# Optimization experiments

Hardware: AMD Instinct MI355X
Metric: run time of the kernel (lower is better)

Reference implementation:

```python
import jax, jax.numpy as jnp
import numpy as np

B, A, T, NMODE, H = 4, 16, 32, 8, 256
NSCENE = 512
HEADS = 8
FF = 128
LN_EPS = 1e-6

def _layer_norm(x, g, b, eps=LN_EPS):
    mu = jnp.mean(x, axis=-1, keepdims=True)
    var = jnp.mean((x - mu) ** 2, axis=-1, keepdims=True)
    return (x - mu) * jax.lax.rsqrt(var + eps) * g + b


def setup_inputs() -> dict:
    key = jax.random.key(0)
    ks = jax.random.split(key, 16)
    s = 1.0 / np.sqrt(H)
    sf = 1.0 / np.sqrt(FF)
    return {
        "hidden_vecs": jax.random.normal(ks[0], (B, A, T, NMODE, H), jnp.float32),
        "scene_hidden_vec": jax.random.normal(ks[1], (B, NSCENE, H), jnp.float32),
        # nn.MultiheadAttention packed in_proj: rows [Wq; Wk; Wv]
        "in_proj_w": jax.random.normal(ks[2], (3 * H, H), jnp.float32) * s,
        "in_proj_b": jnp.zeros((3 * H,), jnp.float32),
        "out_proj_w": jax.random.normal(ks[3], (H, H), jnp.float32) * s,
        "out_proj_b": jnp.zeros((H,), jnp.float32),
        "attn_ln_g": jnp.ones((H,), jnp.float32),
        "attn_ln_b": jnp.zeros((H,), jnp.float32),
        "ff1_w": jax.random.normal(ks[4], (FF, H), jnp.float32) * s,
        "ff1_b": jnp.zeros((FF,), jnp.float32),
        "ff2_w": jax.random.normal(ks[5], (H, FF), jnp.float32) * sf,
        "ff2_b": jnp.zeros((H,), jnp.float32),
        "ff_ln_g": jnp.ones((H,), jnp.float32),
        "ff_ln_b": jnp.zeros((H,), jnp.float32),
    }


def reference(hidden_vecs, scene_hidden_vec, in_proj_w, in_proj_b, out_proj_w,
              out_proj_b, attn_ln_g, attn_ln_b, ff1_w, ff1_b, ff2_w, ff2_b,
              ff_ln_g, ff_ln_b):
    b, a, t, n, h = hidden_vecs.shape
    N = scene_hidden_vec.shape[1]
    d = h // HEADS
    m = a * t * n  # queries per batch element

    Wq, Wk, Wv = in_proj_w[:h], in_proj_w[h:2 * h], in_proj_w[2 * h:]
    bq, bk, bv = in_proj_b[:h], in_proj_b[h:2 * h], in_proj_b[2 * h:]

    # Project queries; K/V computed ONCE per batch (shared across a,t,n) --
    # avoids materializing the (b,a,t,n,N,h) expanded tensor.
    q = (hidden_vecs.reshape(b, m, h) @ Wq.T + bq).reshape(b, m, HEADS, d)
    k = (scene_hidden_vec @ Wk.T + bk).reshape(b, N, HEADS, d)
    v = (scene_hidden_vec @ Wv.T + bv).reshape(b, N, HEADS, d)

    scale = 1.0 / np.sqrt(d)
    scores = jnp.einsum('bmed,bned->bemn', q * scale, k)  # (b, heads, m, N)
    attn = jax.nn.softmax(scores, axis=-1)
    ctx = jnp.einsum('bemn,bned->bmed', attn, v).reshape(b, m, h)
    attn_out = (ctx @ out_proj_w.T + out_proj_b).reshape(b, a, t, n, h)

    # averaged attention weights over heads (average_attn_weights=True)
    attn_score = jnp.mean(attn, axis=1).reshape(b, a, t, n, 1, N)

    x = _layer_norm(attn_out + hidden_vecs, attn_ln_g, attn_ln_b)
    ff = jax.nn.relu(x @ ff1_w.T + ff1_b) @ ff2_w.T + ff2_b
    out = _layer_norm(ff + x, ff_ln_g, ff_ln_b)
    return out, attn_score
```

## Files before the change

### kernel.cpp

```cpp
#include <hip/hip_runtime.h>
#include <hip/hip_bf16.h>

#define H 256
#define NSC 512
#define MQ 4096
#define BATCH 4

typedef __attribute__((ext_vector_type(8))) short bf16x8;
typedef __attribute__((ext_vector_type(4))) float f32x4;

__device__ __forceinline__ ushort f2bf(float x) {
    union { float f; unsigned u; } c; c.f = x;
    unsigned r = c.u + 0x7FFF + ((c.u >> 16) & 1);
    return (ushort)(r >> 16);
}
__device__ __forceinline__ unsigned pk2(float hi, float lo) {
    union { float f; unsigned u; } a, b; a.f = hi; b.f = lo;
    return __builtin_amdgcn_perm(a.u, b.u, 0x07060302u);
}
__device__ __forceinline__ uint4 cvt8f(const float* p) {
    float4 a = *(const float4*)p;
    float4 b = *(const float4*)(p + 4);
    uint4 r;
    r.x = pk2(a.y, a.x); r.y = pk2(a.w, a.z);
    r.z = pk2(b.y, b.x); r.w = pk2(b.w, b.z);
    return r;
}
#define EXP2(x) __builtin_amdgcn_exp2f(x)

template<int ATYPE>
__device__ __forceinline__ uint4 load_a(const void* Ain, size_t off) {
    if (ATYPE == 0) return cvt8f((const float*)Ain + off);
    return *(const uint4*)((const ushort*)Ain + off);
}

template<int ATYPE, int MODE>
__global__ __launch_bounds__(512, 4) void gemm_kernel(
    const void* __restrict__ Ain, const float* __restrict__ W,
    const float* __restrict__ bias, const float* __restrict__ res,
    const float* __restrict__ lng, const float* __restrict__ lnb,
    void* __restrict__ out, ushort* __restrict__ out2,
    int K, int N, float alpha, int relu)
{
    __shared__ ushort As[64 * 64];
    __shared__ ushort Bs[256 * 64];
    __shared__ float Ls[64 * 4];
    __shared__ float Lq[64 * 4];
    const int t = threadIdx.x;
    const int w = t >> 6, lane = t & 63, g = lane >> 4, l15 = lane & 15;
    const int rowBase = blockIdx.y * 64;
    const int colBase = blockIdx.x * 256;
    const int wr = (w >> 2) * 32;
    const int wc = (w & 3) * 64;
    f32x4 acc[2][4];
    #pragma unroll
    for (int mt = 0; mt < 2; mt++)
        #pragma unroll
        for (int nt = 0; nt < 4; nt++) acc[mt][nt] = (f32x4){0.f,0.f,0.f,0.f};

    const int sr = t >> 3, skc = t & 7, sp = skc ^ (sr & 7);
    const size_t arow = (size_t)(rowBase + sr) * K + skc * 8;

    uint4 av = load_a<ATYPE>(Ain, arow);
    uint4 bv[4];
    #pragma unroll
    for (int i = 0; i < 4; i++) {
        const int u = t + 512*i, br = u >> 3, bkc = u & 7;
        int brow = colBase + br; if (brow > N - 1) brow = N - 1;
        bv[i] = cvt8f(W + (size_t)brow * K + bkc*8);
    }

    for (int k0 = 0; k0 < K; k0 += 64) {
        __syncthreads();
        *(uint4*)&As[sr*64 + sp*8] = av;
        #pragma unroll
        for (int i = 0; i < 4; i++) {
            const int u = t + 512*i, br = u >> 3, bkc = u & 7, bp = bkc ^ (br & 7);
            *(uint4*)&Bs[br*64 + bp*8] = bv[i];
        }
        __syncthreads();
        if (k0 + 64 < K) {
            av = load_a<ATYPE>(Ain, arow + k0 + 64);
            #pragma unroll
            for (int i = 0; i < 4; i++) {
                const int u = t + 512*i, br = u >> 3, bkc = u & 7;
                int brow = colBase + br; if (brow > N - 1) brow = N - 1;
                bv[i] = cvt8f(W + (size_t)brow * K + k0 + 64 + bkc*8);
            }
        }
        #pragma unroll
        for (int kk = 0; kk < 2; kk++) {
            const int swz = ((kk*4 + g) ^ (l15 & 7)) * 8;
            bf16x8 af[2], bfr[4];
            #pragma unroll
            for (int mt = 0; mt < 2; mt++)
                af[mt] = *(const bf16x8*)&As[(wr + mt*16 + l15)*64 + swz];
            #pragma unroll
            for (int nt = 0; nt < 4; nt++)
                bfr[nt] = *(const bf16x8*)&Bs[(wc + nt*16 + l15)*64 + swz];
            #pragma unroll
            for (int mt = 0; mt < 2; mt++)
                #pragma unroll
                for (int nt = 0; nt < 4; nt++)
                    acc[mt][nt] = __builtin_amdgcn_mfma_f32_16x16x32_bf16(
                        af[mt], bfr[nt], acc[mt][nt], 0, 0, 0);
        }
    }

    if (MODE == 0) {
        #pragma unroll
        for (int nt = 0; nt < 4; nt++) {
            const int col = colBase + wc + nt*16 + l15;
            if (col < N) {
                const float bb = bias[col];
                #pragma unroll
                for (int mt = 0; mt < 2; mt++)
                    #pragma unroll
                    for (int r = 0; r < 4; r++) {
                        const int row = rowBase + wr + mt*16 + g*4 + r;
                        float o = (acc[mt][nt][r] + bb) * alpha;
                        if (relu) o = fmaxf(o, 0.f);
                        ((ushort*)out)[(size_t)row * N + col] = f2bf(o);
                    }
            }
        }
    } else if (MODE == 1) {
        #pragma unroll
        for (int nt = 0; nt < 4; nt++) {
            const int col = colBase + wc + nt*16 + l15;
            const float bb = bias[col];
            #pragma unroll
            for (int mt = 0; mt < 2; mt++) {
                const int row0 = rowBase + wr + mt*16 + g*4;
                if (col < 256) {
                    #pragma unroll
                    for (int r = 0; r < 4; r++)
                        ((ushort*)out)[(size_t)(row0 + r) * 256 + col] = f2bf(acc[mt][nt][r] + bb);
                } else {
                    ushort4 pkv = { f2bf(acc[mt][nt][0] + bb), f2bf(acc[mt][nt][1] + bb),
                                    f2bf(acc[mt][nt][2] + bb), f2bf(acc[mt][nt][3] + bb) };
                    *(ushort4*)&out2[(size_t)((row0 >> 9)*256 + col - 256) * 512 + (row0 & 511)] = pkv;
                }
            }
        }
    } else {
        float bb[4], gmv[4], btv[4];
        #pragma unroll
        for (int nt = 0; nt < 4; nt++) {
            const int col = wc + nt*16 + l15;
            bb[nt] = bias[col]; gmv[nt] = lng[col]; btv[nt] = lnb[col];
        }
        #pragma unroll
        for (int mt = 0; mt < 2; mt++)
            #pragma unroll
            for (int r = 0; r < 4; r++) {
                const int row = rowBase + wr + mt*16 + g*4 + r;
                const float* rp = res + (size_t)row * 256;
                #pragma unroll
                for (int nt = 0; nt < 4; nt++)
                    acc[mt][nt][r] += bb[nt] + rp[wc + nt*16 + l15];
            }
        float ps[2][4], pq[2][4];
        #pragma unroll
        for (int mt = 0; mt < 2; mt++)
            #pragma unroll
            for (int r = 0; r < 4; r++) {
                float s = (acc[mt][0][r] + acc[mt][1][r]) + (acc[mt][2][r] + acc[mt][3][r]);
                float qq = (acc[mt][0][r]*acc[mt][0][r] + acc[mt][1][r]*acc[mt][1][r])
                         + (acc[mt][2][r]*acc[mt][2][r] + acc[mt][3][r]*acc[mt][3][r]);
                #pragma unroll
                for (int m = 1; m < 16; m <<= 1) {
                    s += __shfl_xor(s, m);
                    qq += __shfl_xor(qq, m);
                }
                ps[mt][r] = s; pq[mt][r] = qq;
            }
        if (l15 == 0) {
            #pragma unroll
            for (int mt = 0; mt < 2; mt++)
                #pragma unroll
                for (int r = 0; r < 4; r++) {
                    const int ri = wr + mt*16 + g*4 + r;
                    Ls[ri*4 + (w & 3)] = ps[mt][r];
                    Lq[ri*4 + (w & 3)] = pq[mt][r];
                }
        }
        __syncthreads();
        #pragma unroll
        for (int mt = 0; mt < 2; mt++)
            #pragma unroll
            for (int r = 0; r < 4; r++) {
                const int ri = wr + mt*16 + g*4 + r;
                const int row = rowBase + ri;
                f32x4 sv = *(const f32x4*)&Ls[ri*4];
                f32x4 qv = *(const f32x4*)&Lq[ri*4];
                const float mu = (sv[0]+sv[1]+sv[2]+sv[3]) * (1.f/256.f);
                const float ex2 = (qv[0]+qv[1]+qv[2]+qv[3]) * (1.f/256.f);
                const float rs = rsqrtf(ex2 - mu*mu + 1e-6f);
                #pragma unroll
                for (int nt = 0; nt < 4; nt++) {
                    const int col = wc + nt*16 + l15;
                    const float o = (acc[mt][nt][r] - mu) * rs * gmv[nt] + btv[nt];
                    ((float*)out)[(size_t)row * 256 + col] = o;
                    if (out2) out2[(size_t)row * 256 + col] = f2bf(o);
                }
            }
    }
}

__global__ __launch_bounds__(512, 2) void ffn_kernel(
    const ushort* __restrict__ ctx, const float* __restrict__ Wo,
    const float* __restrict__ bo, const float* __restrict__ hid,
    const float* __restrict__ ag, const float* __restrict__ ab,
    const float* __restrict__ W1, const float* __restrict__ b1,
    const float* __restrict__ W2, const float* __restrict__ b2,
    const float* __restrict__ fg, const float* __restrict__ fbv,
    float* __restrict__ out)
{
    __shared__ ushort As[64 * 64];
    __shared__ ushort Bs[256 * 64];
    __shared__ ushort Xb[64 * 256];
    __shared__ ushort Fb[64 * 128];
    __shared__ float Ls[64 * 4];
    __shared__ float Lq[64 * 4];

    const int t = threadIdx.x;
    const int w = t >> 6, lane = t & 63, g = lane >> 4, l15 = lane & 15;
    const int rowBase = blockIdx.x * 64;
    const int wr = (w >> 2) * 32;
    const int wc = (w & 3) * 64;
    const int sr = t >> 3, skc = t & 7, sp = skc ^ (sr & 7);

    float xres[2][4][4];

    {
        f32x4 acc[2][4];
        #pragma unroll
        for (int mt = 0; mt < 2; mt++)
            #pragma unroll
            for (int nt = 0; nt < 4; nt++) acc[mt][nt] = (f32x4){0.f,0.f,0.f,0.f};

        uint4 av = *(const uint4*)(ctx + (size_t)(rowBase + sr) * 256 + skc*8);
        uint4 bv[4];
        #pragma unroll
        for (int i = 0; i < 4; i++) {
            const int u = t + 512*i, br = u >> 3, bkc = u & 7;
            bv[i] = cvt8f(Wo + (size_t)br * 256 + bkc*8);
        }
        for (int k0 = 0; k0 < 256; k0 += 64) {
            __syncthreads();
            *(uint4*)&As[sr*64 + sp*8] = av;
            #pragma unroll
            for (int i = 0; i < 4; i++) {
                const int u = t + 512*i, br = u >> 3, bkc = u & 7, bp = bkc ^ (br & 7);
                *(uint4*)&Bs[br*64 + bp*8] = bv[i];
            }
            __syncthreads();
            if (k0 < 192) {
                av = *(const uint4*)(ctx + (size_t)(rowBase + sr) * 256 + k0 + 64 + skc*8);
                #pragma unroll
                for (int i = 0; i < 4; i++) {
                    const int u = t + 512*i, br = u >> 3, bkc = u & 7;
                    bv[i] = cvt8f(Wo + (size_t)br * 256 + k0 + 64 + bkc*8);
                }
            }
            #pragma unroll
            for (int kk = 0; kk < 2; kk++) {
                const int swz = ((kk*4 + g) ^ (l15 & 7)) * 8;
                bf16x8 af[2], bfr[4];
                #pragma unroll
                for (int mt = 0; mt < 2; mt++)
                    af[mt] = *(const bf16x8*)&As[(wr + mt*16 + l15)*64 + swz];
                #pragma unroll
                for (int nt = 0; nt < 4; nt++)
                    bfr[nt] = *(const bf16x8*)&Bs[(wc + nt*16 + l15)*64 + swz];
                #pragma unroll
                for (int mt = 0; mt < 2; mt++)
                    #pragma unroll
                    for (int nt = 0; nt < 4; nt++)
                        acc[mt][nt] = __builtin_amdgcn_mfma_f32_16x16x32_bf16(
                            af[mt], bfr[nt], acc[mt][nt], 0, 0, 0);
            }
        }
        float bb[4], gmv[4], btv[4];
        #pragma unroll
        for (int nt = 0; nt < 4; nt++) {
            const int col = wc + nt*16 + l15;
            bb[nt] = bo[col]; gmv[nt] = ag[col]; btv[nt] = ab[col];
        }
        #pragma unroll
        for (int mt = 0; mt < 2; mt++)
            #pragma unroll
            for (int r = 0; r < 4; r++) {
                const int row = rowBase + wr + mt*16 + g*4 + r;
                const float* rp = hid + (size_t)row * 256;
                #pragma unroll
                for (int nt = 0; nt < 4; nt++)
                    acc[mt][nt][r] += bb[nt] + rp[wc + nt*16 + l15];
            }
        float ps[2][4], pq[2][4];
        #pragma unroll
        for (int mt = 0; mt < 2; mt++)
            #pragma unroll
            for (int r = 0; r < 4; r++) {
                float s = (acc[mt][0][r] + acc[mt][1][r]) + (acc[mt][2][r] + acc[mt][3][r]);
                float qq = (acc[mt][0][r]*acc[mt][0][r] + acc[mt][1][r]*acc[mt][1][r])
                         + (acc[mt][2][r]*acc[mt][2][r] + acc[mt][3][r]*acc[mt][3][r]);
                #pragma unroll
                for (int m = 1; m < 16; m <<= 1) {
                    s += __shfl_xor(s, m);
                    qq += __shfl_xor(qq, m);
                }
                ps[mt][r] = s; pq[mt][r] = qq;
            }
        if (l15 == 0) {
            #pragma unroll
            for (int mt = 0; mt < 2; mt++)
                #pragma unroll
                for (int r = 0; r < 4; r++) {
                    const int ri = wr + mt*16 + g*4 + r;
                    Ls[ri*4 + (w & 3)] = ps[mt][r];
                    Lq[ri*4 + (w & 3)] = pq[mt][r];
                }
        }
        __syncthreads();
        #pragma unroll
        for (int mt = 0; mt < 2; mt++)
            #pragma unroll
            for (int r = 0; r < 4; r++) {
                const int ri = wr + mt*16 + g*4 + r;
                f32x4 sv = *(const f32x4*)&Ls[ri*4];
                f32x4 qv = *(const f32x4*)&Lq[ri*4];
                const float mu = (sv[0]+sv[1]+sv[2]+sv[3]) * (1.f/256.f);
                const float ex2 = (qv[0]+qv[1]+qv[2]+qv[3]) * (1.f/256.f);
                const float rs = rsqrtf(ex2 - mu*mu + 1e-6f);
                #pragma unroll
                for (int nt = 0; nt < 4; nt++) {
                    const int col = wc + nt*16 + l15;
                    const float o = (acc[mt][nt][r] - mu) * rs * gmv[nt] + btv[nt];
                    xres[mt][nt][r * 0 + 0] = xres[mt][nt][0];
                    xres[mt][nt][r] = o;
                    Xb[ri*256 + (((col >> 3) ^ (ri & 7)) << 3) + (col & 7)] = f2bf(o);
                }
            }
    }

    {
        const int wrB = (w >> 1) * 16;
        const int wcB = (w & 1) * 64;
        f32x4 facc[4];
        #pragma unroll
        for (int nt = 0; nt < 4; nt++) facc[nt] = (f32x4){0.f,0.f,0.f,0.f};

        uint4 bv2[2];
        #pragma unroll
        for (int i = 0; i < 2; i++) {
            const int u = t + 512*i, br = u >> 3, bkc = u & 7;
            bv2[i] = cvt8f(W1 + (size_t)br * 256 + bkc*8);
        }
        for (int k0 = 0; k0 < 256; k0 += 64) {
            __syncthreads();
            #pragma unroll
            for (int i = 0; i < 2; i++) {
                const int u = t + 512*i, br = u >> 3, bkc = u & 7, bp = bkc ^ (br & 7);
                *(uint4*)&Bs[br*64 + bp*8] = bv2[i];
            }
            __syncthreads();
            if (k0 < 192) {
                #pragma unroll
                for (int i = 0; i < 2; i++) {
                    const int u = t + 512*i, br = u >> 3, bkc = u & 7;
                    bv2[i] = cvt8f(W1 + (size_t)br * 256 + k0 + 64 + bkc*8);
                }
            }
            #pragma unroll
            for (int kk = 0; kk < 2; kk++) {
                const int rowX = wrB + l15;
                const int gi = (k0 >> 3) + kk*4 + g;
                bf16x8 af = *(const bf16x8*)&Xb[rowX*256 + ((gi ^ (rowX & 7)) << 3)];
                const int swz = ((kk*4 + g) ^ (l15 & 7)) * 8;
                #pragma unroll
                for (int nt = 0; nt < 4; nt++) {
                    bf16x8 bfr = *(const bf16x8*)&Bs[(wcB + nt*16 + l15)*64 + swz];
                    facc[nt] = __builtin_amdgcn_mfma_f32_16x16x32_bf16(
                        af, bfr, facc[nt], 0, 0, 0);
                }
            }
        }
        #pragma unroll
        for (int nt = 0; nt < 4; nt++) {
            const int colF = wcB + nt*16 + l15;
            const float fbb = b1[colF];
            #pragma unroll
            for (int r = 0; r < 4; r++) {
                const int rowF = wrB + g*4 + r;
                const float o = fmaxf(facc[nt][r] + fbb, 0.f);
                Fb[rowF*128 + (((colF >> 3) ^ (rowF & 7)) << 3) + (colF & 7)] = f2bf(o);
            }
        }
        __syncthreads();
    }

    {
        f32x4 acc2[2][4];
        #pragma unroll
        for (int mt = 0; mt < 2; mt++)
            #pragma unroll
            for (int nt = 0; nt < 4; nt++) acc2[mt][nt] = (f32x4){0.f,0.f,0.f,0.f};

        uint4 bv3[4];
        #pragma unroll
        for (int i = 0; i < 4; i++) {
            const int u = t + 512*i, br = u >> 3, bkc = u & 7;
            bv3[i] = cvt8f(W2 + (size_t)br * 128 + bkc*8);
        }
        for (int k0 = 0; k0 < 128; k0 += 64) {
            __syncthreads();
            #pragma unroll
            for (int i = 0; i < 4; i++) {
                const int u = t + 512*i, br = u >> 3, bkc = u & 7, bp = bkc ^ (br & 7);
                *(uint4*)&Bs[br*64 + bp*8] = bv3[i];
            }
            __syncthreads();
            if (k0 == 0) {
                #pragma unroll
                for (int i = 0; i < 4; i++) {
                    const int u = t + 512*i, br = u >> 3, bkc = u & 7;
                    bv3[i] = cvt8f(W2 + (size_t)br * 128 + 64 + bkc*8);
                }
            }
            #pragma unroll
            for (int kk = 0; kk < 2; kk++) {
                const int gi = (k0 >> 3) + kk*4 + g;
                bf16x8 af2[2], bfr[4];
                #pragma unroll
                for (int mt = 0; mt < 2; mt++) {
                    const int rowF = wr + mt*16 + l15;
                    af2[mt] = *(const bf16x8*)&Fb[rowF*128 + ((gi ^ (rowF & 7)) << 3)];
                }
                const int swz = ((kk*4 + g) ^ (l15 & 7)) * 8;
                #pragma unroll
                for (int nt = 0; nt < 4; nt++)
                    bfr[nt] = *(const bf16x8*)&Bs[(wc + nt*16 + l15)*64 + swz];
                #pragma unroll
                for (int mt = 0; mt < 2; mt++)
                    #pragma unroll
                    for (int nt = 0; nt < 4; nt++)
                        acc2[mt][nt] = __builtin_amdgcn_mfma_f32_16x16x32_bf16(
                            af2[mt], bfr[nt], acc2[mt][nt], 0, 0, 0);
            }
        }
        float bb[4], gmv[4], btv[4];
        #pragma unroll
        for (int nt = 0; nt < 4; nt++) {
            const int col = wc + nt*16 + l15;
            bb[nt] = b2[col]; gmv[nt] = fg[col]; btv[nt] = fbv[col];
        }
        #pragma unroll
        for (int mt = 0; mt < 2; mt++)
            #pragma unroll
            for (int r = 0; r < 4; r++)
                #pragma unroll
                for (int nt = 0; nt < 4; nt++)
                    acc2[mt][nt][r] += bb[nt] + xres[mt][nt][r];
        float ps[2][4], pq[2][4];
        #pragma unroll
        for (int mt = 0; mt < 2; mt++)
            #pragma unroll
            for (int r = 0; r < 4; r++) {
                float s = (acc2[mt][0][r] + acc2[mt][1][r]) + (acc2[mt][2][r] + acc2[mt][3][r]);
                float qq = (acc2[mt][0][r]*acc2[mt][0][r] + acc2[mt][1][r]*acc2[mt][1][r])
                         + (acc2[mt][2][r]*acc2[mt][2][r] + acc2[mt][3][r]*acc2[mt][3][r]);
                #pragma unroll
                for (int m = 1; m < 16; m <<= 1) {
                    s += __shfl_xor(s, m);
                    qq += __shfl_xor(qq, m);
                }
                ps[mt][r] = s; pq[mt][r] = qq;
            }
        __syncthreads();
        if (l15 == 0) {
            #pragma unroll
            for (int mt = 0; mt < 2; mt++)
                #pragma unroll
                for (int r = 0; r < 4; r++) {
                    const int ri = wr + mt*16 + g*4 + r;
                    Ls[ri*4 + (w & 3)] = ps[mt][r];
                    Lq[ri*4 + (w & 3)] = pq[mt][r];
                }
        }
        __syncthreads();
        #pragma unroll
        for (int mt = 0; mt < 2; mt++)
            #pragma unroll
            for (int r = 0; r < 4; r++) {
                const int ri = wr + mt*16 + g*4 + r;
                const int row = rowBase + ri;
                f32x4 sv = *(const f32x4*)&Ls[ri*4];
                f32x4 qv = *(const f32x4*)&Lq[ri*4];
                const float mu = (sv[0]+sv[1]+sv[2]+sv[3]) * (1.f/256.f);
                const float ex2 = (qv[0]+qv[1]+qv[2]+qv[3]) * (1.f/256.f);
                const float rs = rsqrtf(ex2 - mu*mu + 1e-6f);
                #pragma unroll
                for (int nt = 0; nt < 4; nt++) {
                    const int col = wc + nt*16 + l15;
                    out[(size_t)row * 256 + col] =
                        (acc2[mt][nt][r] - mu) * rs * gmv[nt] + btv[nt];
                }
            }
    }
}

__global__ __launch_bounds__(512, 4) void attn_kernel(
    const ushort* __restrict__ q, const ushort* __restrict__ k,
    const ushort* __restrict__ vt, ushort* __restrict__ ctx_out,
    float* __restrict__ attn_score)
{
    __shared__ ushort Ks[32 * 264];
    __shared__ ushort Vs[256 * 40];
    __shared__ ushort Pb[8 * 32 * 40];
    __shared__ float Lg[256];
    const int t = threadIdx.x;
    const int w = t >> 6;
    const int lane = t & 63;
    const int g = lane >> 4;
    const int l15 = lane & 15;
    const int b = blockIdx.x >> 7;
    const int m0 = (blockIdx.x & 127) * 32;

    const size_t kg = (size_t)b * NSC * H;
    const size_t vg = (size_t)b * H * NSC;

    bf16x8 qf[2];
    #pragma unroll
    for (int qt = 0; qt < 2; qt++)
        qf[qt] = *(const bf16x8*)&q[((size_t)(b*MQ + m0 + qt*16 + l15)) * H + w*32 + g*8];

    f32x4 cacc[2][2];
    float lacc[2][4];
    #pragma unroll
    for (int qt = 0; qt < 2; qt++) {
        #pragma unroll
        for (int dt = 0; dt < 2; dt++) cacc[qt][dt] = (f32x4){0.f,0.f,0.f,0.f};
        #pragma unroll
        for (int r = 0; r < 4; r++) lacc[qt][r] = 0.f;
    }

    bf16x8 kr[2], vr[2];
    #pragma unroll
    for (int i = 0; i < 2; i++) {
        const int u = t + 512*i;
        const int key = u >> 5, part = u & 31;
        kr[i] = *(const bf16x8*)&k[kg + (size_t)key*H + part*8];
        const int d = u >> 2, p2 = u & 3;
        vr[i] = *(const bf16x8*)&vt[vg + (size_t)d*NSC + p2*8];
    }

    for (int c = 0; c < 16; c++) {
        const int kbase = c * 32;
        __syncthreads();
        #pragma unroll
        for (int i = 0; i < 2; i++) {
            const int u = t + 512*i;
            const int key = u >> 5, part = u & 31;
            *(bf16x8*)&Ks[key*264 + part*8] = kr[i];
            const int d = u >> 2, p2 = u & 3;
            *(bf16x8*)&Vs[d*40 + p2*8] = vr[i];
        }
        __syncthreads();
        if (c < 15) {
            #pragma unroll
            for (int i = 0; i < 2; i++) {
                const int u = t + 512*i;
                const int key = u >> 5, part = u & 31;
                kr[i] = *(const bf16x8*)&k[kg + (size_t)(kbase + 32 + key)*H + part*8];
                const int d = u >> 2, p2 = u & 3;
                vr[i] = *(const bf16x8*)&vt[vg + (size_t)d*NSC + kbase + 32 + p2*8];
            }
        }
        #pragma unroll
        for (int qt = 0; qt < 2; qt++) {
            #pragma unroll
            for (int kt = 0; kt < 2; kt++) {
                bf16x8 kf = *(const bf16x8*)&Ks[(kt*16 + l15)*264 + w*32 + g*8];
                f32x4 s = __builtin_amdgcn_mfma_f32_16x16x32_bf16(
                    qf[qt], kf, (f32x4){0.f,0.f,0.f,0.f}, 0, 0, 0);
                #pragma unroll
                for (int r = 0; r < 4; r++) {
                    float p = EXP2(s[r]);
                    lacc[qt][r] += p;
                    Pb[(w*32 + qt*16 + g*4 + r)*40 + kt*16 + l15] = f2bf(p);
                }
            }
        }
        #pragma unroll
        for (int qt = 0; qt < 2; qt++) {
            bf16x8 pf = *(const bf16x8*)&Pb[(w*32 + qt*16 + l15)*40 + g*8];
            #pragma unroll
            for (int dt = 0; dt < 2; dt++) {
                bf16x8 vf = *(const bf16x8*)&Vs[(w*32 + dt*16 + l15)*40 + g*8];
                cacc[qt][dt] = __builtin_amdgcn_mfma_f32_16x16x32_bf16(
                    pf, vf, cacc[qt][dt], 0, 0, 0);
            }
        }
    }

    #pragma unroll
    for (int qt = 0; qt < 2; qt++) {
        float invl[4];
        #pragma unroll
        for (int r = 0; r < 4; r++) {
            float v = lacc[qt][r];
            v += __shfl_xor(v, 1); v += __shfl_xor(v, 2);
            v += __shfl_xor(v, 4); v += __shfl_xor(v, 8);
            invl[r] = 1.f / v;
            if (l15 == 0) Lg[w*32 + qt*16 + g*4 + r] = -__log2f(v) - 3.0f;
        }
        #pragma unroll
        for (int dt = 0; dt < 2; dt++)
            #pragma unroll
            for (int r = 0; r < 4; r++)
                ctx_out[((size_t)(b*MQ + m0 + qt*16 + g*4 + r))*H + w*32 + dt*16 + l15]
                    = f2bf(cacc[qt][dt][r] * invl[r]);
    }

    __syncthreads();

    f32x4 sacc[2][4];
    #pragma unroll
    for (int qt = 0; qt < 2; qt++)
        #pragma unroll
        for (int kt = 0; kt < 4; kt++) sacc[qt][kt] = (f32x4){0.f,0.f,0.f,0.f};

    #pragma unroll 2
    for (int h = 0; h < 8; h++) {
        const float lg0 = Lg[h*32 + l15];
        const float lg1 = Lg[h*32 + 16 + l15];
        bf16x8 q0 = *(const bf16x8*)&q[((size_t)(b*MQ + m0 + l15)) * H + h*32 + g*8];
        bf16x8 q1 = *(const bf16x8*)&q[((size_t)(b*MQ + m0 + 16 + l15)) * H + h*32 + g*8];
        #pragma unroll
        for (int kt = 0; kt < 4; kt++) {
            bf16x8 kf = *(const bf16x8*)&k[kg + (size_t)(w*64 + kt*16 + l15)*H + h*32 + g*8];
            f32x4 s0 = __builtin_amdgcn_mfma_f32_16x16x32_bf16(
                kf, q0, (f32x4){0.f,0.f,0.f,0.f}, 0, 0, 0);
            #pragma unroll
            for (int r = 0; r < 4; r++) sacc[0][kt][r] += EXP2(s0[r] + lg0);
            f32x4 s1 = __builtin_amdgcn_mfma_f32_16x16x32_bf16(
                kf, q1, (f32x4){0.f,0.f,0.f,0.f}, 0, 0, 0);
            #pragma unroll
            for (int r = 0; r < 4; r++) sacc[1][kt][r] += EXP2(s1[r] + lg1);
        }
    }
    #pragma unroll
    for (int qt = 0; qt < 2; qt++)
        #pragma unroll
        for (int kt = 0; kt < 4; kt++)
            *(f32x4*)&attn_score[((size_t)(b*MQ + m0 + qt*16 + l15))*NSC + w*64 + kt*16 + g*4]
                = sacc[qt][kt];
}

extern "C" void kernel_launch(void* const* d_in, const int* in_sizes, int n_in,
                              void* d_out, int out_size, void* d_ws, size_t ws_size,
                              hipStream_t stream)
{
    const float* hidden = (const float*)d_in[0];
    const float* scene  = (const float*)d_in[1];
    const float* in_w   = (const float*)d_in[2];
    const float* in_b   = (const float*)d_in[3];
    const float* out_w  = (const float*)d_in[4];
    const float* out_b  = (const float*)d_in[5];
    const float* aln_g  = (const float*)d_in[6];
    const float* aln_b  = (const float*)d_in[7];
    const float* ff1_w  = (const float*)d_in[8];
    const float* ff1_b  = (const float*)d_in[9];
    const float* ff2_w  = (const float*)d_in[10];
    const float* ff2_b  = (const float*)d_in[11];
    const float* fln_g  = (const float*)d_in[12];
    const float* fln_b  = (const float*)d_in[13];

    float* out0  = (float*)d_out;
    float* score = out0 + (size_t)BATCH * MQ * H;

    ushort* qb   = (ushort*)d_ws;
    ushort* kb   = qb   + 4194304;
    ushort* vtb  = kb   + 524288;
    ushort* ctxb = vtb  + 524288;

    const float alpha_q = 0.25507609683638066f;
    dim3 blk(512);

    gemm_kernel<0,0><<<dim3(1,256), blk, 0, stream>>>(
        hidden, in_w, in_b, nullptr, nullptr, nullptr, qb, nullptr, 256, 256, alpha_q, 0);
    gemm_kernel<0,1><<<dim3(2,32), blk, 0, stream>>>(
        scene, in_w + 65536, in_b + 256, nullptr, nullptr, nullptr, kb, vtb, 256, 512, 1.f, 0);
    attn_kernel<<<dim3(512), blk, 0, stream>>>(qb, kb, vtb, ctxb, score);
    ffn_kernel<<<dim3(256), blk, 0, stream>>>(
        ctxb, out_w, out_b, hidden, aln_g, aln_b,
        ff1_w, ff1_b, ff2_w, ff2_b, fln_g, fln_b, out0);
}
```

Before: 193.7 us.

## Merge Q and KV projections into one launch and widen FFN blocks to 1024 threads

The separate Q-projection and K/V-projection GEMM launches become a single kernel whose block index selects the Q or KV path, which removes one launch and lets both GEMMs run concurrently. The fused FFN kernel now uses 1024-thread blocks with 16 waves, each owning a 16-row slice instead of 32 rows. This cuts per-thread accumulator registers and gives more waves per block to hide latency. In exchange there is more per-wave LDS fragment traffic relative to MFMA work, and only half the threads load the A tile.

```diff
diff --git a/kernel.cpp b/kernel.cpp
--- a/kernel.cpp
+++ b/kernel.cpp
@@ -28,28 +28,18 @@
 }
 #define EXP2(x) __builtin_amdgcn_exp2f(x)
 
-template<int ATYPE>
-__device__ __forceinline__ uint4 load_a(const void* Ain, size_t off) {
-    if (ATYPE == 0) return cvt8f((const float*)Ain + off);
-    return *(const uint4*)((const ushort*)Ain + off);
-}
-
-template<int ATYPE, int MODE>
-__global__ __launch_bounds__(512, 4) void gemm_kernel(
-    const void* __restrict__ Ain, const float* __restrict__ W,
-    const float* __restrict__ bias, const float* __restrict__ res,
-    const float* __restrict__ lng, const float* __restrict__ lnb,
+template<int MODE>
+__device__ __forceinline__ void gemm_body(
+    ushort* As, ushort* Bs, int bx, int by,
+    const float* __restrict__ Ain, const float* __restrict__ W,
+    const float* __restrict__ bias,
     void* __restrict__ out, ushort* __restrict__ out2,
-    int K, int N, float alpha, int relu)
+    int K, int N, float alpha)
 {
-    __shared__ ushort As[64 * 64];
-    __shared__ ushort Bs[256 * 64];
-    __shared__ float Ls[64 * 4];
-    __shared__ float Lq[64 * 4];
     const int t = threadIdx.x;
     const int w = t >> 6, lane = t & 63, g = lane >> 4, l15 = lane & 15;
-    const int rowBase = blockIdx.y * 64;
-    const int colBase = blockIdx.x * 256;
+    const int rowBase = by * 64;
+    const int colBase = bx * 256;
     const int wr = (w >> 2) * 32;
     const int wc = (w & 3) * 64;
     f32x4 acc[2][4];
@@ -61,7 +51,7 @@
     const int sr = t >> 3, skc = t & 7, sp = skc ^ (sr & 7);
     const size_t arow = (size_t)(rowBase + sr) * K + skc * 8;
 
-    uint4 av = load_a<ATYPE>(Ain, arow);
+    uint4 av = cvt8f(Ain + arow);
     uint4 bv[4];
     #pragma unroll
     for (int i = 0; i < 4; i++) {
@@ -80,7 +70,7 @@
         }
         __syncthreads();
         if (k0 + 64 < K) {
-            av = load_a<ATYPE>(Ain, arow + k0 + 64);
+            av = cvt8f(Ain + arow + k0 + 64);
             #pragma unroll
             for (int i = 0; i < 4; i++) {
                 const int u = t + 512*i, br = u >> 3, bkc = u & 7;
@@ -119,12 +109,11 @@
                     for (int r = 0; r < 4; r++) {
                         const int row = rowBase + wr + mt*16 + g*4 + r;
                         float o = (acc[mt][nt][r] + bb) * alpha;
-                        if (relu) o = fmaxf(o, 0.f);
                         ((ushort*)out)[(size_t)row * N + col] = f2bf(o);
                     }
             }
         }
-    } else if (MODE == 1) {
+    } else {
         #pragma unroll
         for (int nt = 0; nt < 4; nt++) {
             const int col = colBase + wc + nt*16 + l15;
@@ -143,72 +132,28 @@
                 }
             }
         }
+    }
+}
+
+__global__ __launch_bounds__(512, 4) void qkv_kernel(
+    const float* __restrict__ hidden, const float* __restrict__ scene,
+    const float* __restrict__ in_w, const float* __restrict__ in_b,
+    ushort* __restrict__ qb, ushort* __restrict__ kb, ushort* __restrict__ vtb,
+    float alpha_q)
+{
+    __shared__ ushort As[64 * 64];
+    __shared__ ushort Bs[256 * 64];
+    if (blockIdx.x < 256) {
+        gemm_body<0>(As, Bs, 0, blockIdx.x, hidden, in_w, in_b,
+                     qb, nullptr, 256, 256, alpha_q);
     } else {
-        float bb[4], gmv[4], btv[4];
-        #pragma unroll
-        for (int nt = 0; nt < 4; nt++) {
-            const int col = wc + nt*16 + l15;
-            bb[nt] = bias[col]; gmv[nt] = lng[col]; btv[nt] = lnb[col];
-        }
-        #pragma unroll
-        for (int mt = 0; mt < 2; mt++)
-            #pragma unroll
-            for (int r = 0; r < 4; r++) {
-                const int row = rowBase + wr + mt*16 + g*4 + r;
-                const float* rp = res + (size_t)row * 256;
-                #pragma unroll
-                for (int nt = 0; nt < 4; nt++)
-                    acc[mt][nt][r] += bb[nt] + rp[wc + nt*16 + l15];
-            }
-        float ps[2][4], pq[2][4];
-        #pragma unroll
-        for (int mt = 0; mt < 2; mt++)
-            #pragma unroll
-            for (int r = 0; r < 4; r++) {
-                float s = (acc[mt][0][r] + acc[mt][1][r]) + (acc[mt][2][r] + acc[mt][3][r]);
-                float qq = (acc[mt][0][r]*acc[mt][0][r] + acc[mt][1][r]*acc[mt][1][r])
-                         + (acc[mt][2][r]*acc[mt][2][r] + acc[mt][3][r]*acc[mt][3][r]);
-                #pragma unroll
-                for (int m = 1; m < 16; m <<= 1) {
-                    s += __shfl_xor(s, m);
-                    qq += __shfl_xor(qq, m);
-                }
-                ps[mt][r] = s; pq[mt][r] = qq;
-            }
-        if (l15 == 0) {
-            #pragma unroll
-            for (int mt = 0; mt < 2; mt++)
-                #pragma unroll
-                for (int r = 0; r < 4; r++) {
-                    const int ri = wr + mt*16 + g*4 + r;
-                    Ls[ri*4 + (w & 3)] = ps[mt][r];
-                    Lq[ri*4 + (w & 3)] = pq[mt][r];
-                }
-        }
-        __syncthreads();
-        #pragma unroll
-        for (int mt = 0; mt < 2; mt++)
-            #pragma unroll
-            for (int r = 0; r < 4; r++) {
-                const int ri = wr + mt*16 + g*4 + r;
-                const int row = rowBase + ri;
-                f32x4 sv = *(const f32x4*)&Ls[ri*4];
-                f32x4 qv = *(const f32x4*)&Lq[ri*4];
-                const float mu = (sv[0]+sv[1]+sv[2]+sv[3]) * (1.f/256.f);
-                const float ex2 = (qv[0]+qv[1]+qv[2]+qv[3]) * (1.f/256.f);
-                const float rs = rsqrtf(ex2 - mu*mu + 1e-6f);
-                #pragma unroll
-                for (int nt = 0; nt < 4; nt++) {
-                    const int col = wc + nt*16 + l15;
-                    const float o = (acc[mt][nt][r] - mu) * rs * gmv[nt] + btv[nt];
-                    ((float*)out)[(size_t)row * 256 + col] = o;
-                    if (out2) out2[(size_t)row * 256 + col] = f2bf(o);
-                }
-            }
-    }
-}
-
-__global__ __launch_bounds__(512, 2) void ffn_kernel(
+        const int bid = blockIdx.x - 256;
+        gemm_body<1>(As, Bs, bid >> 5, bid & 31, scene, in_w + 65536, in_b + 256,
+                     kb, vtb, 256, 512, 1.f);
+    }
+}
+
+__global__ __launch_bounds__(1024, 4) void ffn_kernel(
     const ushort* __restrict__ ctx, const float* __restrict__ Wo,
     const float* __restrict__ bo, const float* __restrict__ hid,
     const float* __restrict__ ag, const float* __restrict__ ab,
@@ -227,59 +172,53 @@
     const int t = threadIdx.x;
     const int w = t >> 6, lane = t & 63, g = lane >> 4, l15 = lane & 15;
     const int rowBase = blockIdx.x * 64;
-    const int wr = (w >> 2) * 32;
+    const int wr = (w >> 2) * 16;
     const int wc = (w & 3) * 64;
     const int sr = t >> 3, skc = t & 7, sp = skc ^ (sr & 7);
 
-    float xres[2][4][4];
+    float xres[4][4];
 
     {
-        f32x4 acc[2][4];
-        #pragma unroll
-        for (int mt = 0; mt < 2; mt++)
-            #pragma unroll
-            for (int nt = 0; nt < 4; nt++) acc[mt][nt] = (f32x4){0.f,0.f,0.f,0.f};
-
-        uint4 av = *(const uint4*)(ctx + (size_t)(rowBase + sr) * 256 + skc*8);
-        uint4 bv[4];
-        #pragma unroll
-        for (int i = 0; i < 4; i++) {
-            const int u = t + 512*i, br = u >> 3, bkc = u & 7;
+        f32x4 acc[4];
+        #pragma unroll
+        for (int nt = 0; nt < 4; nt++) acc[nt] = (f32x4){0.f,0.f,0.f,0.f};
+
+        uint4 av;
+        if (t < 512) av = *(const uint4*)(ctx + (size_t)(rowBase + sr) * 256 + skc*8);
+        uint4 bv[2];
+        #pragma unroll
+        for (int i = 0; i < 2; i++) {
+            const int u = t + 1024*i, br = u >> 3, bkc = u & 7;
             bv[i] = cvt8f(Wo + (size_t)br * 256 + bkc*8);
         }
         for (int k0 = 0; k0 < 256; k0 += 64) {
             __syncthreads();
-            *(uint4*)&As[sr*64 + sp*8] = av;
-            #pragma unroll
-            for (int i = 0; i < 4; i++) {
-                const int u = t + 512*i, br = u >> 3, bkc = u & 7, bp = bkc ^ (br & 7);
+            if (t < 512) *(uint4*)&As[sr*64 + sp*8] = av;
+            #pragma unroll
+            for (int i = 0; i < 2; i++) {
+                const int u = t + 1024*i, br = u >> 3, bkc = u & 7, bp = bkc ^ (br & 7);
                 *(uint4*)&Bs[br*64 + bp*8] = bv[i];
             }
             __syncthreads();
             if (k0 < 192) {
-                av = *(const uint4*)(ctx + (size_t)(rowBase + sr) * 256 + k0 + 64 + skc*8);
-                #pragma unroll
-                for (int i = 0; i < 4; i++) {
-                    const int u = t + 512*i, br = u >> 3, bkc = u & 7;
+                if (t < 512)
+                    av = *(const uint4*)(ctx + (size_t)(rowBase + sr) * 256 + k0 + 64 + skc*8);
+                #pragma unroll
+                for (int i = 0; i < 2; i++) {
+                    const int u = t + 1024*i, br = u >> 3, bkc = u & 7;
                     bv[i] = cvt8f(Wo + (size_t)br * 256 + k0 + 64 + bkc*8);
                 }
             }
             #pragma unroll
             for (int kk = 0; kk < 2; kk++) {
                 const int swz = ((kk*4 + g) ^ (l15 & 7)) * 8;
-                bf16x8 af[2], bfr[4];
-                #pragma unroll
-                for (int mt = 0; mt < 2; mt++)
-                    af[mt] = *(const bf16x8*)&As[(wr + mt*16 + l15)*64 + swz];
-                #pragma unroll
-                for (int nt = 0; nt < 4; nt++)
-                    bfr[nt] = *(const bf16x8*)&Bs[(wc + nt*16 + l15)*64 + swz];
-                #pragma unroll
-                for (int mt = 0; mt < 2; mt++)
-                    #pragma unroll
-                    for (int nt = 0; nt < 4; nt++)
-                        acc[mt][nt] = __builtin_amdgcn_mfma_f32_16x16x32_bf16(
-                            af[mt], bfr[nt], acc[mt][nt], 0, 0, 0);
+                bf16x8 af = *(const bf16x8*)&As[(wr + l15)*64 + swz];
+                #pragma unroll
+                for (int nt = 0; nt < 4; nt++) {
+                    bf16x8 bfr = *(const bf16x8*)&Bs[(wc + nt*16 + l15)*64 + swz];
+                    acc[nt] = __builtin_amdgcn_mfma_f32_16x16x32_bf16(
+                        af, bfr, acc[nt], 0, 0, 0);
+                }
             }
         }
         float bb[4], gmv[4], btv[4];
@@ -289,90 +228,70 @@
             bb[nt] = bo[col]; gmv[nt] = ag[col]; btv[nt] = ab[col];
         }
         #pragma unroll
-        for (int mt = 0; mt < 2; mt++)
+        for (int r = 0; r < 4; r++) {
+            const int row = rowBase + wr + g*4 + r;
+            const float* rp = hid + (size_t)row * 256;
+            #pragma unroll
+            for (int nt = 0; nt < 4; nt++)
+                acc[nt][r] += bb[nt] + rp[wc + nt*16 + l15];
+        }
+        float ps[4], pq[4];
+        #pragma unroll
+        for (int r = 0; r < 4; r++) {
+            float s = (acc[0][r] + acc[1][r]) + (acc[2][r] + acc[3][r]);
+            float qq = (acc[0][r]*acc[0][r] + acc[1][r]*acc[1][r])
+                     + (acc[2][r]*acc[2][r] + acc[3][r]*acc[3][r]);
+            #pragma unroll
+            for (int m = 1; m < 16; m <<= 1) {
+                s += __shfl_xor(s, m);
+                qq += __shfl_xor(qq, m);
+            }
+            ps[r] = s; pq[r] = qq;
+        }
+        if (l15 == 0) {
             #pragma unroll
             for (int r = 0; r < 4; r++) {
-                const int row = rowBase + wr + mt*16 + g*4 + r;
-                const float* rp = hid + (size_t)row * 256;
-                #pragma unroll
-                for (int nt = 0; nt < 4; nt++)
-                    acc[mt][nt][r] += bb[nt] + rp[wc + nt*16 + l15];
-            }
-        float ps[2][4], pq[2][4];
-        #pragma unroll
-        for (int mt = 0; mt < 2; mt++)
-            #pragma unroll
-            for (int r = 0; r < 4; r++) {
-                float s = (acc[mt][0][r] + acc[mt][1][r]) + (acc[mt][2][r] + acc[mt][3][r]);
-                float qq = (acc[mt][0][r]*acc[mt][0][r] + acc[mt][1][r]*acc[mt][1][r])
-                         + (acc[mt][2][r]*acc[mt][2][r] + acc[mt][3][r]*acc[mt][3][r]);
-                #pragma unroll
-                for (int m = 1; m < 16; m <<= 1) {
-                    s += __shfl_xor(s, m);
-                    qq += __shfl_xor(qq, m);
-                }
-                ps[mt][r] = s; pq[mt][r] = qq;
-            }
-        if (l15 == 0) {
-            #pragma unroll
-            for (int mt = 0; mt < 2; mt++)
-                #pragma unroll
-                for (int r = 0; r < 4; r++) {
-                    const int ri = wr + mt*16 + g*4 + r;
-                    Ls[ri*4 + (w & 3)] = ps[mt][r];
-                    Lq[ri*4 + (w & 3)] = pq[mt][r];
-                }
-        }
-        __syncthreads();
-        #pragma unroll
-        for (int mt = 0; mt < 2; mt++)
-            #pragma unroll
-            for (int r = 0; r < 4; r++) {
-                const int ri = wr + mt*16 + g*4 + r;
-                f32x4 sv = *(const f32x4*)&Ls[ri*4];
-                f32x4 qv = *(const f32x4*)&Lq[ri*4];
-                const float mu = (sv[0]+sv[1]+sv[2]+sv[3]) * (1.f/256.f);
-                const float ex2 = (qv[0]+qv[1]+qv[2]+qv[3]) * (1.f/256.f);
-                const float rs = rsqrtf(ex2 - mu*mu + 1e-6f);
-                #pragma unroll
-                for (int nt = 0; nt < 4; nt++) {
-                    const int col = wc + nt*16 + l15;
-                    const float o = (acc[mt][nt][r] - mu) * rs * gmv[nt] + btv[nt];
-                    xres[mt][nt][r * 0 + 0] = xres[mt][nt][0];
-                    xres[mt][nt][r] = o;
-                    Xb[ri*256 + (((col >> 3) ^ (ri & 7)) << 3) + (col & 7)] = f2bf(o);
-                }
-            }
+                const int ri = wr + g*4 + r;
+                Ls[ri*4 + (w & 3)] = ps[r];
+                Lq[ri*4 + (w & 3)] = pq[r];
+            }
+        }
+        __syncthreads();
+        #pragma unroll
+        for (int r = 0; r < 4; r++) {
+            const int ri = wr + g*4 + r;
+            f32x4 sv = *(const f32x4*)&Ls[ri*4];
+            f32x4 qv = *(const f32x4*)&Lq[ri*4];
+            const float mu = (sv[0]+sv[1]+sv[2]+sv[3]) * (1.f/256.f);
+            const float ex2 = (qv[0]+qv[1]+qv[2]+qv[3]) * (1.f/256.f);
+            const float rs = rsqrtf(ex2 - mu*mu + 1e-6f);
+            #pragma unroll
+            for (int nt = 0; nt < 4; nt++) {
+                const int col = wc + nt*16 + l15;
+                const float o = (acc[nt][r] - mu) * rs * gmv[nt] + btv[nt];
+                xres[nt][r] = o;
+                Xb[ri*256 + (((col >> 3) ^ (ri & 7)) << 3) + (col & 7)] = f2bf(o);
+            }
+        }
     }
 
     {
-        const int wrB = (w >> 1) * 16;
-        const int wcB = (w & 1) * 64;
-        f32x4 facc[4];
-        #pragma unroll
-        for (int nt = 0; nt < 4; nt++) facc[nt] = (f32x4){0.f,0.f,0.f,0.f};
-
-        uint4 bv2[2];
-        #pragma unroll
-        for (int i = 0; i < 2; i++) {
-            const int u = t + 512*i, br = u >> 3, bkc = u & 7;
-            bv2[i] = cvt8f(W1 + (size_t)br * 256 + bkc*8);
-        }
+        const int wrB = (w >> 2) * 16;
+        const int wcB = (w & 3) * 32;
+        f32x4 facc[2];
+        #pragma unroll
+        for (int nt = 0; nt < 2; nt++) facc[nt] = (f32x4){0.f,0.f,0.f,0.f};
+
+        uint4 bv2 = cvt8f(W1 + (size_t)(t >> 3) * 256 + (t & 7)*8);
         for (int k0 = 0; k0 < 256; k0 += 64) {
             __syncthreads();
-            #pragma unroll
-            for (int i = 0; i < 2; i++) {
-                const int u = t + 512*i, br = u >> 3, bkc = u & 7, bp = bkc ^ (br & 7);
-                *(uint4*)&Bs[br*64 + bp*8] = bv2[i];
+            {
+                const int br = t >> 3, bkc = t & 7, bp = bkc ^ (br & 7);
+                *(uint4*)&Bs[br*64 + bp*8] = bv2;
             }
             __syncthreads();
-            if (k0 < 192) {
-                #pragma unroll
-                for (int i = 0; i < 2; i++) {
-                    const int u = t + 512*i, br = u >> 3, bkc = u & 7;
-                    bv2[i] = cvt8f(W1 + (size_t)br * 256 + k0 + 64 + bkc*8);
-                }
-            }
+            if (k0 < 192)
+                bv2 = cvt8f(W1 + (size_t)(t >> 3) * 256 + k0 + 64 + (t & 7)*8);
             #pragma unroll
             for (int kk = 0; kk < 2; kk++) {
                 const int rowX = wrB + l15;
@@ -380,7 +299,7 @@
                 bf16x8 af = *(const bf16x8*)&Xb[rowX*256 + ((gi ^ (rowX & 7)) << 3)];
                 const int swz = ((kk*4 + g) ^ (l15 & 7)) * 8;
                 #pragma unroll
-                for (int nt = 0; nt < 4; nt++) {
+                for (int nt = 0; nt < 2; nt++) {
                     bf16x8 bfr = *(const bf16x8*)&Bs[(wcB + nt*16 + l15)*64 + swz];
                     facc[nt] = __builtin_amdgcn_mfma_f32_16x16x32_bf16(
                         af, bfr, facc[nt], 0, 0, 0);
@@ -388,7 +307,7 @@
             }
         }
         #pragma unroll
-        for (int nt = 0; nt < 4; nt++) {
+        for (int nt = 0; nt < 2; nt++) {
             const int colF = wcB + nt*16 + l15;
             const float fbb = b1[colF];
             #pragma unroll
@@ -402,52 +321,43 @@
     }
 
     {
-        f32x4 acc2[2][4];
-        #pragma unroll
-        for (int mt = 0; mt < 2; mt++)
-            #pragma unroll
-            for (int nt = 0; nt < 4; nt++) acc2[mt][nt] = (f32x4){0.f,0.f,0.f,0.f};
-
-        uint4 bv3[4];
-        #pragma unroll
-        for (int i = 0; i < 4; i++) {
-            const int u = t + 512*i, br = u >> 3, bkc = u & 7;
+        f32x4 acc2[4];
+        #pragma unroll
+        for (int nt = 0; nt < 4; nt++) acc2[nt] = (f32x4){0.f,0.f,0.f,0.f};
+
+        uint4 bv3[2];
+        #pragma unroll
+        for (int i = 0; i < 2; i++) {
+            const int u = t + 1024*i, br = u >> 3, bkc = u & 7;
             bv3[i] = cvt8f(W2 + (size_t)br * 128 + bkc*8);
         }
         for (int k0 = 0; k0 < 128; k0 += 64) {
             __syncthreads();
             #pragma unroll
-            for (int i = 0; i < 4; i++) {
-                const int u = t + 512*i, br = u >> 3, bkc = u & 7, bp = bkc ^ (br & 7);
+            for (int i = 0; i < 2; i++) {
+                const int u = t + 1024*i, br = u >> 3, bkc = u & 7, bp = bkc ^ (br & 7);
                 *(uint4*)&Bs[br*64 + bp*8] = bv3[i];
             }
             __syncthreads();
             if (k0 == 0) {
                 #pragma unroll
-                for (int i = 0; i < 4; i++) {
-                    const int u = t + 512*i, br = u >> 3, bkc = u & 7;
+                for (int i = 0; i < 2; i++) {
+                    const int u = t + 1024*i, br = u >> 3, bkc = u & 7;
                     bv3[i] = cvt8f(W2 + (size_t)br * 128 + 64 + bkc*8);
                 }
             }
             #pragma unroll
             for (int kk = 0; kk < 2; kk++) {
                 const int gi = (k0 >> 3) + kk*4 + g;
-                bf16x8 af2[2], bfr[4];
-                #pragma unroll
-                for (int mt = 0; mt < 2; mt++) {
-                    const int rowF = wr + mt*16 + l15;
-                    af2[mt] = *(const bf16x8*)&Fb[rowF*128 + ((gi ^ (rowF & 7)) << 3)];
-                }
+                const int rowF = wr + l15;
+                bf16x8 af2 = *(const bf16x8*)&Fb[rowF*128 + ((gi ^ (rowF & 7)) << 3)];
                 const int swz = ((kk*4 + g) ^ (l15 & 7)) * 8;
                 #pragma unroll
-                for (int nt = 0; nt < 4; nt++)
-                    bfr[nt] = *(const bf16x8*)&Bs[(wc + nt*16 + l15)*64 + swz];
-                #pragma unroll
-                for (int mt = 0; mt < 2; mt++)
-                    #pragma unroll
-                    for (int nt = 0; nt < 4; nt++)
-                        acc2[mt][nt] = __builtin_amdgcn_mfma_f32_16x16x32_bf16(
-                            af2[mt], bfr[nt], acc2[mt][nt], 0, 0, 0);
+                for (int nt = 0; nt < 4; nt++) {
+                    bf16x8 bfr = *(const bf16x8*)&Bs[(wc + nt*16 + l15)*64 + swz];
+                    acc2[nt] = __builtin_amdgcn_mfma_f32_16x16x32_bf16(
+                        af2, bfr, acc2[nt], 0, 0, 0);
+                }
             }
         }
         float bb[4], gmv[4], btv[4];
@@ -457,57 +367,49 @@
             bb[nt] = b2[col]; gmv[nt] = fg[col]; btv[nt] = fbv[col];
         }
         #pragma unroll
-        for (int mt = 0; mt < 2; mt++)
-            #pragma unroll
-            for (int r = 0; r < 4; r++)
-                #pragma unroll
-                for (int nt = 0; nt < 4; nt++)
-                    acc2[mt][nt][r] += bb[nt] + xres[mt][nt][r];
-        float ps[2][4], pq[2][4];
-        #pragma unroll
-        for (int mt = 0; mt < 2; mt++)
+        for (int r = 0; r < 4; r++)
+            #pragma unroll
+            for (int nt = 0; nt < 4; nt++)
+                acc2[nt][r] += bb[nt] + xres[nt][r];
+        float ps[4], pq[4];
+        #pragma unroll
+        for (int r = 0; r < 4; r++) {
+            float s = (acc2[0][r] + acc2[1][r]) + (acc2[2][r] + acc2[3][r]);
+            float qq = (acc2[0][r]*acc2[0][r] + acc2[1][r]*acc2[1][r])
+                     + (acc2[2][r]*acc2[2][r] + acc2[3][r]*acc2[3][r]);
+            #pragma unroll
+            for (int m = 1; m < 16; m <<= 1) {
+                s += __shfl_xor(s, m);
+                qq += __shfl_xor(qq, m);
+            }
+            ps[r] = s; pq[r] = qq;
+        }
+        __syncthreads();
+        if (l15 == 0) {
             #pragma unroll
             for (int r = 0; r < 4; r++) {
-                float s = (acc2[mt][0][r] + acc2[mt][1][r]) + (acc2[mt][2][r] + acc2[mt][3][r]);
-                float qq = (acc2[mt][0][r]*acc2[mt][0][r] + acc2[mt][1][r]*acc2[mt][1][r])
-                         + (acc2[mt][2][r]*acc2[mt][2][r] + acc2[mt][3][r]*acc2[mt][3][r]);
-                #pragma unroll
-                for (int m = 1; m < 16; m <<= 1) {
-                    s += __shfl_xor(s, m);
-                    qq += __shfl_xor(qq, m);
-                }
-                ps[mt][r] = s; pq[mt][r] = qq;
-            }
-        __syncthreads();
-        if (l15 == 0) {
-            #pragma unroll
-            for (int mt = 0; mt < 2; mt++)
-                #pragma unroll
-                for (int r = 0; r < 4; r++) {
-                    const int ri = wr + mt*16 + g*4 + r;
-                    Ls[ri*4 + (w & 3)] = ps[mt][r];
-                    Lq[ri*4 + (w & 3)] = pq[mt][r];
-                }
-        }
-        __syncthreads();
-        #pragma unroll
-        for (int mt = 0; mt < 2; mt++)
-            #pragma unroll
-            for (int r = 0; r < 4; r++) {
-                const int ri = wr + mt*16 + g*4 + r;
-                const int row = rowBase + ri;
-                f32x4 sv = *(const f32x4*)&Ls[ri*4];
-                f32x4 qv = *(const f32x4*)&Lq[ri*4];
-                const float mu = (sv[0]+sv[1]+sv[2]+sv[3]) * (1.f/256.f);
-                const float ex2 = (qv[0]+qv[1]+qv[2]+qv[3]) * (1.f/256.f);
-                const float rs = rsqrtf(ex2 - mu*mu + 1e-6f);
-                #pragma unroll
-                for (int nt = 0; nt < 4; nt++) {
-                    const int col = wc + nt*16 + l15;
-                    out[(size_t)row * 256 + col] =
-                        (acc2[mt][nt][r] - mu) * rs * gmv[nt] + btv[nt];
-                }
-            }
+                const int ri = wr + g*4 + r;
+                Ls[ri*4 + (w & 3)] = ps[r];
+                Lq[ri*4 + (w & 3)] = pq[r];
+            }
+        }
+        __syncthreads();
+        #pragma unroll
+        for (int r = 0; r < 4; r++) {
+            const int ri = wr + g*4 + r;
+            const int row = rowBase + ri;
+            f32x4 sv = *(const f32x4*)&Ls[ri*4];
+            f32x4 qv = *(const f32x4*)&Lq[ri*4];
+            const float mu = (sv[0]+sv[1]+sv[2]+sv[3]) * (1.f/256.f);
+            const float ex2 = (qv[0]+qv[1]+qv[2]+qv[3]) * (1.f/256.f);
+            const float rs = rsqrtf(ex2 - mu*mu + 1e-6f);
+            #pragma unroll
+            for (int nt = 0; nt < 4; nt++) {
+                const int col = wc + nt*16 + l15;
+                out[(size_t)row * 256 + col] =
+                    (acc2[nt][r] - mu) * rs * gmv[nt] + btv[nt];
+            }
+        }
     }
 }
 
@@ -687,14 +589,11 @@
     ushort* ctxb = vtb  + 524288;
 
     const float alpha_q = 0.25507609683638066f;
-    dim3 blk(512);
-
-    gemm_kernel<0,0><<<dim3(1,256), blk, 0, stream>>>(
-        hidden, in_w, in_b, nullptr, nullptr, nullptr, qb, nullptr, 256, 256, alpha_q, 0);
-    gemm_kernel<0,1><<<dim3(2,32), blk, 0, stream>>>(
-        scene, in_w + 65536, in_b + 256, nullptr, nullptr, nullptr, kb, vtb, 256, 512, 1.f, 0);
-    attn_kernel<<<dim3(512), blk, 0, stream>>>(qb, kb, vtb, ctxb, score);
-    ffn_kernel<<<dim3(256), blk, 0, stream>>>(
+
+    qkv_kernel<<<dim3(320), dim3(512), 0, stream>>>(
+        hidden, scene, in_w, in_b, qb, kb, vtb, alpha_q);
+    attn_kernel<<<dim3(512), dim3(512), 0, stream>>>(qb, kb, vtb, ctxb, score);
+    ffn_kernel<<<dim3(256), dim3(1024), 0, stream>>>(
         ctxb, out_w, out_b, hidden, aln_g, aln_b,
         ff1_w, ff1_b, ff2_w, ff2_b, fln_g, fln_b, out0);
 }
```

Result: faster. 185.0 us (-4.5%).
